# Kernel optimization log

Hardware: AMD Instinct MI355X
Metric: run time of the kernel (lower is better)

The kernel has to match this reference:

```python
import jax, jax.numpy as jnp
import numpy as np
from jax import lax

NE_RATIO = 0.8
SCALING_G = 1.0
W_FF = 30.0
SIG_EXT = 5.0
VT = 20.0
VR = 0.0
DT = 1e-3
NMAX = 60  # fixed Euler step count (Euler2fixedpt)
CONTRASTS = [0.0, 0.0432773, 0.103411, 0.186966, 0.303066, 0.464386, 0.68854, 1.0]
ORIENTS = [0., 15., 30., 45., 60., 75., 90., 105., 120., 135., 150., 165.]

# f_ricci polynomial coeffs in (-z), highest degree first (a9..a1, 0)
_FA = np.array([.14805913578876898, .64290613877355551, 1.0616084849547165,
                .93524391761244940, .62718906618071668, .32171431660633076,
                .32056016125642045, .77373949685442023, .22757881388024176, 0.0],
               dtype=np.float32)

def f_ricci(x):
    z = x / (1.0 + x)
    return jnp.log(2.0 * x + 1.0) + jnp.polyval(jnp.asarray(_FA), -z)

def g_ricci(x):
    z = x / (2.0 + x)
    num = z * (3.5441754117462949 + z * (-7.0529131065835378 + z * (-56.532378057580381
          + z * (279.56761105465944 + z * (-520.37554849441472 + z * (456.58245777026514
          + z * (-155.73340457809226)))))))
    den = 1.0 + z * (-4.1357968834226053 + z * (-7.2984226138266743 + z * (98.656602235468327
          + z * (-334.20436223415163 + z * (601.08633903294185 + z * (-599.58577549598340
          + z * (277.18420330693891 + z * (-16.445022798669722))))))))
    return num / den

def phi(mu, sigma, tau, tau_ref):
    """Ricciardi LIF transfer (Sanzeni rational approximation), branch-safe for jit."""
    xp = (mu - VR) / sigma
    xm = (mu - VT) / sigma
    cA = xm > 0
    cB = (xm <= 0) & (xp > 0)
    cC = xp <= 0
    xmA = jnp.where(cA, xm, 1.0); xpA = jnp.where(cA, xp, 2.0)
    rA = 1.0 / (f_ricci(xpA) - f_ricci(xmA))
    xmB = jnp.where(cB, xm, -1.0); xpB = jnp.where(cB, xp, 1.0)
    rB = 1.0 / (f_ricci(xpB) + jnp.exp(xmB * xmB) * g_ricci(-xmB))
    xmC = jnp.where(cC, xm, -2.0); xpC = jnp.where(cC, xp, -1.0)
    rC = jnp.exp(-xmC * xmC - jnp.log(g_ricci(-xmC) - jnp.exp(xpC * xpC - xmC * xmC) * g_ricci(-xpC)))
    r0 = jnp.where(cA, rA, jnp.where(cB, rB, rC))
    r0 = jnp.maximum(r0, 1e-30)
    return 1.0 / (tau_ref + tau / r0)

def _forward(hyperparameters, rand_mat, N):
    Ne = int(N * NE_RATIO); Ni = N - Ne
    pref = jnp.concatenate([
        jnp.linspace(0.0, 179.99, Ne, endpoint=False, dtype=jnp.float32),
        jnp.linspace(0.0, 179.99, Ni, endpoint=False, dtype=jnp.float32)])
    diff = jnp.abs(pref[:, None] - pref[None, :])              # [N,N]
    is_i = (jnp.arange(N) >= Ne).astype(jnp.int32)
    conn = is_i[:, None] + 2 * is_i[None, :]                   # 0:EE 1:IE 2:EI 3:II
    J = hyperparameters[0][conn]
    P = hyperparameters[1][conn]
    W = hyperparameters[2][conn]
    z = jnp.exp((jnp.cos(2.0 * jnp.pi / 180.0 * diff) - 1.0) / (4.0 * (jnp.pi / 180.0 * W) ** 2))
    weights = J * jax.nn.sigmoid(32.0 * (P * z - rand_mat))    # [N,N]
    weights2 = weights * weights
    tau = jnp.concatenate([0.01 * jnp.ones(Ne, jnp.float32), 0.01 * jnp.ones(Ni, jnp.float32)])
    T_inv = jnp.concatenate([100.0 * jnp.ones(Ne, jnp.float32), 200.0 * jnp.ones(Ni, jnp.float32)])
    tau_ref = jnp.concatenate([0.005 * jnp.ones(Ne, jnp.float32), 0.001 * jnp.ones(Ni, jnp.float32)])
    contrasts = jnp.asarray(CONTRASTS, jnp.float32)
    orients = jnp.asarray(ORIENTS, jnp.float32)
    dth = orients[None, :, None] - pref[None, None, :]         # [1,12,N]
    cg = jnp.exp((jnp.cos(2.0 * jnp.pi / 180.0 * dth) - 1.0) / (4.0 * (jnp.pi / 180.0 * W_FF) ** 2))
    mean = (contrasts[:, None, None] * 20.0 * SCALING_G * cg).reshape(-1, N)  # [96,N]
    sd2 = SIG_EXT * SIG_EXT

    def step(rate, _):
        mu = tau * (rate @ weights.T) + mean                   # [96,N]
        sig = jnp.sqrt(tau * (rate @ weights2.T) + sd2)
        rate = rate + DT * T_inv * (phi(mu, sig, tau, tau_ref) - rate)
        return rate, None

    rate, _ = lax.scan(step, jnp.zeros_like(mean), None, length=NMAX)
    all_rates = rate.reshape(len(CONTRASTS), len(ORIENTS), N)
    return jnp.transpose(all_rates, (2, 0, 1))                 # [N, 8, 12]

def setup_inputs():
    key = jax.random.key(0)
    hyperparameters = jnp.array([[1.99, 1.9, -1.01, -0.79],
                                 [0.11, 0.11, 0.45, 0.45],
                                 [32.0, 32.0, 32.0, 32.0]], dtype=jnp.float32)
    rand_mat = jax.random.uniform(key, (1500, 1500), dtype=jnp.float32)
    return {"hyperparameters": hyperparameters, "rand_mat": rand_mat, "neuron_num": 1500}

def reference(hyperparameters, rand_mat, neuron_num):
    return _forward(hyperparameters, rand_mat, neuron_num)
```

## Files before the change

kernel.cpp:

```cpp
#include <hip/hip_runtime.h>
#include <hip/hip_bf16.h>
#include <math.h>

#define NN      1500
#define NEE     1200
#define NPAD    1536
#define BATCH   96
#define NSTEP   60
#define PI_F    3.14159265358979323846f

#define NTHR    1024
#define WAVES   16
#define KSLW    (NPAD / WAVES)
#define BH      48
#define MFR     3

#define BP      49
#define SLOTF   (2 * 16 * BP)
#define LDS_BYTES (WAVES * SLOTF * 4)

typedef __attribute__((ext_vector_type(8))) short short8b;
typedef __attribute__((ext_vector_type(4))) float f32x4;


__device__ __forceinline__ ushort bf16_rn(float x) {
    unsigned u = __float_as_uint(x);
    unsigned r = (u + 0x7FFFu + ((u >> 16) & 1u)) >> 16;
    return (ushort)r;
}
__device__ __forceinline__ float bf16f(ushort h) {
    return __uint_as_float(((unsigned)h) << 16);
}


__device__ __forceinline__ float f_ricci(float x) {
    float z = x / (1.0f + x);
    float t = -z;
    float p = 0.14805913578876898f;
    p = p * t + 0.64290613877355551f;
    p = p * t + 1.0616084849547165f;
    p = p * t + 0.93524391761244940f;
    p = p * t + 0.62718906618071668f;
    p = p * t + 0.32171431660633076f;
    p = p * t + 0.32056016125642045f;
    p = p * t + 0.77373949685442023f;
    p = p * t + 0.22757881388024176f;
    p = p * t;
    return logf(2.0f * x + 1.0f) + p;
}

__device__ __forceinline__ float g_ricci(float x) {
    float z = x / (2.0f + x);
    float num = z * (3.5441754117462949f + z * (-7.0529131065835378f + z * (-56.532378057580381f
        + z * (279.56761105465944f + z * (-520.37554849441472f + z * (456.58245777026514f
        + z * (-155.73340457809226f)))))));
    float den = 1.0f + z * (-4.1357968834226053f + z * (-7.2984226138266743f + z * (98.656602235468327f
        + z * (-334.20436223415163f + z * (601.08633903294185f + z * (-599.58577549598340f
        + z * (277.18420330693891f + z * (-16.445022798669722f))))))));
    return num / den;
}

__device__ __forceinline__ float phi_lif(float mu, float sig, float tau, float tau_ref) {
    float xp = mu / sig;
    float xm = (mu - 20.0f) / sig;
    float r0;
    if (xm > 0.0f) {
        r0 = 1.0f / (f_ricci(xp) - f_ricci(xm));
    } else if (xp > 0.0f) {
        r0 = 1.0f / (f_ricci(xp) + expf(xm * xm) * g_ricci(-xm));
    } else {
        float a = g_ricci(-xm) - expf(xp * xp - xm * xm) * g_ricci(-xp);
        r0 = expf(-xm * xm - logf(a));
    }
    r0 = fmaxf(r0, 1e-30f);
    return 1.0f / (tau_ref + tau / r0);
}

__device__ __forceinline__ float pref_of(int n) {
    const float stepE = 179.99f / 1200.0f;
    const float stepI = 179.99f / 300.0f;
    return (n < NEE) ? (float)n * stepE : (float)(n - NEE) * stepI;
}


__global__ __launch_bounds__(256) void k_weights(const float* __restrict__ hyp,
        const float* __restrict__ rand_mat,
        ushort* __restrict__ Whi, ushort* __restrict__ Wlo,
        ushort* __restrict__ W2hi, ushort* __restrict__ W2lo) {
    int k = blockIdx.x * 256 + threadIdx.x;
    int i = blockIdx.y;
    size_t idx = (size_t)i * NPAD + k;
    if (i >= NN || k >= NN) {
        Whi[idx] = 0; Wlo[idx] = 0; W2hi[idx] = 0; W2lo[idx] = 0;
        return;
    }
    float diff = fabsf(pref_of(i) - pref_of(k));
    int conn = (i >= NEE ? 1 : 0) + 2 * (k >= NEE ? 1 : 0);
    float J  = hyp[conn];
    float P  = hyp[4 + conn];
    float Wp = hyp[8 + conn];
    float dn = 4.0f * (PI_F / 180.0f * Wp) * (PI_F / 180.0f * Wp);
    float z = expf((cosf(2.0f * PI_F / 180.0f * diff) - 1.0f) / dn);
    float x = 32.0f * (P * z - rand_mat[(size_t)i * NN + k]);
    float w = J / (1.0f + expf(-x));
    float w2 = w * w;
    ushort h = bf16_rn(w);
    Whi[idx] = h;  Wlo[idx] = bf16_rn(w - bf16f(h));
    ushort h2 = bf16_rn(w2);
    W2hi[idx] = h2; W2lo[idx] = bf16_rn(w2 - bf16f(h2));
}


__global__ __launch_bounds__(256) void k_init(float* __restrict__ mean,
                                              float* __restrict__ rate,
                                              ushort* __restrict__ rhiA,
                                              ushort* __restrict__ rloA) {
    int i = blockIdx.x * 256 + threadIdx.x;
    int b = blockIdx.y;
    int c = b / 12, o = b % 12;
    const float contrasts[8] = {0.0f, 0.0432773f, 0.103411f, 0.186966f,
                                0.303066f, 0.464386f, 0.68854f, 1.0f};
    float m = 0.0f;
    if (i < NN) {
        float dth = 15.0f * (float)o - pref_of(i);
        const float dn = 4.0f * (PI_F / 180.0f * 30.0f) * (PI_F / 180.0f * 30.0f);
        m = contrasts[c] * 20.0f * expf((cosf(2.0f * PI_F / 180.0f * dth) - 1.0f) / dn);
    }
    size_t idx = (size_t)b * NPAD + i;
    mean[idx] = m;
    rate[idx] = 0.0f;
    rhiA[idx] = 0;
    rloA[idx] = 0;
}


__global__ __launch_bounds__(NTHR) void k_step(
        const ushort* __restrict__ Whi, const ushort* __restrict__ Wlo,
        const ushort* __restrict__ W2hi, const ushort* __restrict__ W2lo,
        const ushort* __restrict__ rin_hi, const ushort* __restrict__ rin_lo,
        ushort* __restrict__ rout_hi, ushort* __restrict__ rout_lo,
        float* __restrict__ rate, const float* __restrict__ mean,
        float* __restrict__ out, int last)
{
    extern __shared__ float sm[];
    const int tid  = threadIdx.x;
    const int wave = tid >> 6;
    const int lane = tid & 63;
    const int lr   = lane & 15;
    const int lq   = lane >> 4;
    const int bx   = blockIdx.x;
    const int it   = bx % 96;
    const int bhf  = bx / 96;
    const int i0   = it * 16;
    const int b0   = bhf * BH;
    const int kb   = wave * KSLW;

    f32x4 acc1[MFR], acc2[MFR];
#pragma unroll
    for (int m = 0; m < MFR; m++) {
        acc1[m] = (f32x4){0.0f, 0.0f, 0.0f, 0.0f};
        acc2[m] = (f32x4){0.0f, 0.0f, 0.0f, 0.0f};
    }

    const size_t bof = (size_t)(i0 + lr) * NPAD + kb + lq * 8;
#pragma unroll
    for (int kk = 0; kk < KSLW / 32; kk++) {
        const int ko = kk * 32;
        short8b wh  = *(const short8b*)(Whi  + bof + ko);
        short8b wl  = *(const short8b*)(Wlo  + bof + ko);
        short8b w2h = *(const short8b*)(W2hi + bof + ko);
        short8b w2l = *(const short8b*)(W2lo + bof + ko);
#pragma unroll
        for (int m = 0; m < MFR; m++) {
            const size_t aof = (size_t)(b0 + m * 16 + lr) * NPAD + kb + lq * 8 + ko;
            short8b ah = *(const short8b*)(rin_hi + aof);
            short8b al = *(const short8b*)(rin_lo + aof);
            acc1[m] = __builtin_amdgcn_mfma_f32_16x16x32_bf16(ah, wh,  acc1[m], 0, 0, 0);
            acc1[m] = __builtin_amdgcn_mfma_f32_16x16x32_bf16(ah, wl,  acc1[m], 0, 0, 0);
            acc1[m] = __builtin_amdgcn_mfma_f32_16x16x32_bf16(al, wh,  acc1[m], 0, 0, 0);
            acc2[m] = __builtin_amdgcn_mfma_f32_16x16x32_bf16(ah, w2h, acc2[m], 0, 0, 0);
            acc2[m] = __builtin_amdgcn_mfma_f32_16x16x32_bf16(ah, w2l, acc2[m], 0, 0, 0);
            acc2[m] = __builtin_amdgcn_mfma_f32_16x16x32_bf16(al, w2h, acc2[m], 0, 0, 0);
        }
    }

    {
        float* sp = sm + wave * SLOTF;
#pragma unroll
        for (int m = 0; m < MFR; m++) {
            float* p1 = sp + lr * BP + m * 16 + 4 * lq;
            float* p2 = p1 + 16 * BP;
            *(f32x4*)p1 = acc1[m];
            *(f32x4*)p2 = acc2[m];
        }
    }
    __syncthreads();

    if (tid < BH * 16) {
        const int c = tid & 15;
        const int b = tid >> 4;
        const int ig = i0 + c;
        const int gb = b0 + b;
        const size_t gx = (size_t)gb * NPAD + ig;
        float rn = 0.0f;
        if (ig < NN) {
            float u1 = 0.0f, u2 = 0.0f;
#pragma unroll
            for (int s = 0; s < WAVES; s++) {
                u1 += sm[s * SLOTF + c * BP + b];
                u2 += sm[s * SLOTF + (16 + c) * BP + b];
            }
            float mu = 0.01f * u1 + mean[gx];
            float sg = sqrtf(0.01f * u2 + 25.0f);
            float tr = (ig < NEE) ? 0.005f : 0.001f;
            float Ti = (ig < NEE) ? 100.0f : 200.0f;
            float rr = rate[gx];
            float ph = phi_lif(mu, sg, 0.01f, tr);
            rn = rr + 1e-3f * Ti * (ph - rr);
            rate[gx] = rn;
            if (last) out[(size_t)ig * BATCH + gb] = rn;
        }
        ushort h = bf16_rn(rn);
        rout_hi[gx] = h;
        rout_lo[gx] = bf16_rn(rn - bf16f(h));
    }
}


extern "C" void kernel_launch(void* const* d_in, const int* in_sizes, int n_in,
                              void* d_out, int out_size, void* d_ws, size_t ws_size,
                              hipStream_t stream) {
    const float* hyp      = (const float*)d_in[0];
    const float* rand_mat = (const float*)d_in[1];
    float* out            = (float*)d_out;

    char* p = (char*)d_ws;
    ushort* Whi  = (ushort*)p; p += (size_t)NPAD * NPAD * 2;
    ushort* Wlo  = (ushort*)p; p += (size_t)NPAD * NPAD * 2;
    ushort* W2hi = (ushort*)p; p += (size_t)NPAD * NPAD * 2;
    ushort* W2lo = (ushort*)p; p += (size_t)NPAD * NPAD * 2;
    ushort* rhiA = (ushort*)p; p += (size_t)BATCH * NPAD * 2;
    ushort* rloA = (ushort*)p; p += (size_t)BATCH * NPAD * 2;
    ushort* rhiB = (ushort*)p; p += (size_t)BATCH * NPAD * 2;
    ushort* rloB = (ushort*)p; p += (size_t)BATCH * NPAD * 2;
    float*  mean = (float*)p;  p += (size_t)BATCH * NPAD * 4;
    float*  rate = (float*)p;  p += (size_t)BATCH * NPAD * 4;

    hipFuncSetAttribute((const void*)k_step,
                        hipFuncAttributeMaxDynamicSharedMemorySize, LDS_BYTES);

    k_weights<<<dim3(NPAD / 256, NPAD), 256, 0, stream>>>(hyp, rand_mat, Whi, Wlo, W2hi, W2lo);
    k_init<<<dim3(NPAD / 256, BATCH), 256, 0, stream>>>(mean, rate, rhiA, rloA);

    for (int s = 0; s < NSTEP; s++) {
        const ushort* ih = (s & 1) ? rhiB : rhiA;
        const ushort* il = (s & 1) ? rloB : rloA;
        ushort* oh = (s & 1) ? rhiA : rhiB;
        ushort* ol = (s & 1) ? rloA : rloB;
        k_step<<<dim3(192), dim3(NTHR), LDS_BYTES, stream>>>(
            Whi, Wlo, W2hi, W2lo, ih, il, oh, ol, rate, mean, out,
            (s == NSTEP - 1) ? 1 : 0);
    }
}
```

Before: 1.175 ms.

## Fuse all Euler steps into one cooperative persistent kernel with group barriers

Replaces the 60 per-step kernel launches with a single cooperative kernel that loops over steps. Workgroups handling the same batch half synchronise through an atomic counter barrier. The rate state and the mean input now live in registers instead of global arrays. Rate planes are read with relaxed agent-scope atomic loads and written as packed 32-bit atomic stores. This removes launch overhead and the per-step global traffic for rate and mean, at the cost of spin-wait barriers and weaker load vectorisation from the split 32-bit atomic loads.

After: 2.345 ms. 99.5% more time.

```diff
diff --git a/kernel.cpp b/kernel.cpp
--- a/kernel.cpp
+++ b/kernel.cpp
@@ -9,6 +9,8 @@
 #define NSTEP   60
 #define PI_F    3.14159265358979323846f
 
+#define NWG     192
+#define GRPWG   96
 #define NTHR    1024
 #define WAVES   16
 #define KSLW    (NPAD / WAVES)
@@ -30,6 +32,16 @@
 }
 __device__ __forceinline__ float bf16f(ushort h) {
     return __uint_as_float(((unsigned)h) << 16);
+}
+
+__device__ __forceinline__ short8b load_pair8(const ushort* plane, size_t elem) {
+    uint* p = (uint*)(plane + elem);
+    union { uint u[4]; short8b v; } x;
+    x.u[0] = __hip_atomic_load(p + 0, __ATOMIC_RELAXED, __HIP_MEMORY_SCOPE_AGENT);
+    x.u[1] = __hip_atomic_load(p + 1, __ATOMIC_RELAXED, __HIP_MEMORY_SCOPE_AGENT);
+    x.u[2] = __hip_atomic_load(p + 2, __ATOMIC_RELAXED, __HIP_MEMORY_SCOPE_AGENT);
+    x.u[3] = __hip_atomic_load(p + 3, __ATOMIC_RELAXED, __HIP_MEMORY_SCOPE_AGENT);
+    return x.v;
 }
 
 
@@ -111,36 +123,24 @@
 }
 
 
-__global__ __launch_bounds__(256) void k_init(float* __restrict__ mean,
-                                              float* __restrict__ rate,
-                                              ushort* __restrict__ rhiA,
-                                              ushort* __restrict__ rloA) {
+__global__ __launch_bounds__(256) void k_init(ushort* __restrict__ rhiA,
+                                              ushort* __restrict__ rloA,
+                                              uint* __restrict__ cnt) {
     int i = blockIdx.x * 256 + threadIdx.x;
     int b = blockIdx.y;
-    int c = b / 12, o = b % 12;
-    const float contrasts[8] = {0.0f, 0.0432773f, 0.103411f, 0.186966f,
-                                0.303066f, 0.464386f, 0.68854f, 1.0f};
-    float m = 0.0f;
-    if (i < NN) {
-        float dth = 15.0f * (float)o - pref_of(i);
-        const float dn = 4.0f * (PI_F / 180.0f * 30.0f) * (PI_F / 180.0f * 30.0f);
-        m = contrasts[c] * 20.0f * expf((cosf(2.0f * PI_F / 180.0f * dth) - 1.0f) / dn);
-    }
     size_t idx = (size_t)b * NPAD + i;
-    mean[idx] = m;
-    rate[idx] = 0.0f;
     rhiA[idx] = 0;
     rloA[idx] = 0;
-}
-
-
-__global__ __launch_bounds__(NTHR) void k_step(
+    if (blockIdx.x == 0 && blockIdx.y == 0 && threadIdx.x < 2) cnt[threadIdx.x] = 0;
+}
+
+
+__global__ __launch_bounds__(NTHR) void k_coop(
         const ushort* __restrict__ Whi, const ushort* __restrict__ Wlo,
         const ushort* __restrict__ W2hi, const ushort* __restrict__ W2lo,
-        const ushort* __restrict__ rin_hi, const ushort* __restrict__ rin_lo,
-        ushort* __restrict__ rout_hi, ushort* __restrict__ rout_lo,
-        float* __restrict__ rate, const float* __restrict__ mean,
-        float* __restrict__ out, int last)
+        ushort* __restrict__ rhiA, ushort* __restrict__ rloA,
+        ushort* __restrict__ rhiB, ushort* __restrict__ rloB,
+        uint* __restrict__ cnt, float* __restrict__ out)
 {
     extern __shared__ float sm[];
     const int tid  = threadIdx.x;
@@ -155,74 +155,115 @@
     const int b0   = bhf * BH;
     const int kb   = wave * KSLW;
 
-    f32x4 acc1[MFR], acc2[MFR];
-#pragma unroll
-    for (int m = 0; m < MFR; m++) {
-        acc1[m] = (f32x4){0.0f, 0.0f, 0.0f, 0.0f};
-        acc2[m] = (f32x4){0.0f, 0.0f, 0.0f, 0.0f};
+    const int c  = tid & 15;
+    const int bb = tid >> 4;
+    const int ig = i0 + c;
+    const int gb = b0 + bb;
+    const size_t gx = (size_t)gb * NPAD + ig;
+    const bool upd = (tid < BH * 16);
+
+    const float contrasts[8] = {0.0f, 0.0432773f, 0.103411f, 0.186966f,
+                                0.303066f, 0.464386f, 0.68854f, 1.0f};
+    const float dnff = 4.0f * (PI_F / 180.0f * 30.0f) * (PI_F / 180.0f * 30.0f);
+    float mean0 = 0.0f;
+    if (upd && ig < NN) {
+        float dth = 15.0f * (float)(gb % 12) - pref_of(ig);
+        mean0 = contrasts[gb / 12] * 20.0f *
+                expf((cosf(2.0f * PI_F / 180.0f * dth) - 1.0f) / dnff);
     }
+    float rr = 0.0f;
 
     const size_t bof = (size_t)(i0 + lr) * NPAD + kb + lq * 8;
-#pragma unroll
-    for (int kk = 0; kk < KSLW / 32; kk++) {
-        const int ko = kk * 32;
-        short8b wh  = *(const short8b*)(Whi  + bof + ko);
-        short8b wl  = *(const short8b*)(Wlo  + bof + ko);
-        short8b w2h = *(const short8b*)(W2hi + bof + ko);
-        short8b w2l = *(const short8b*)(W2lo + bof + ko);
+
+    for (int s = 0; s < NSTEP; s++) {
+        const ushort* rin_hi = (s & 1) ? rhiB : rhiA;
+        const ushort* rin_lo = (s & 1) ? rloB : rloA;
+        ushort* rout_hi = (s & 1) ? rhiA : rhiB;
+        ushort* rout_lo = (s & 1) ? rloA : rloB;
+
+        f32x4 acc1[MFR], acc2[MFR];
 #pragma unroll
         for (int m = 0; m < MFR; m++) {
-            const size_t aof = (size_t)(b0 + m * 16 + lr) * NPAD + kb + lq * 8 + ko;
-            short8b ah = *(const short8b*)(rin_hi + aof);
-            short8b al = *(const short8b*)(rin_lo + aof);
-            acc1[m] = __builtin_amdgcn_mfma_f32_16x16x32_bf16(ah, wh,  acc1[m], 0, 0, 0);
-            acc1[m] = __builtin_amdgcn_mfma_f32_16x16x32_bf16(ah, wl,  acc1[m], 0, 0, 0);
-            acc1[m] = __builtin_amdgcn_mfma_f32_16x16x32_bf16(al, wh,  acc1[m], 0, 0, 0);
-            acc2[m] = __builtin_amdgcn_mfma_f32_16x16x32_bf16(ah, w2h, acc2[m], 0, 0, 0);
-            acc2[m] = __builtin_amdgcn_mfma_f32_16x16x32_bf16(ah, w2l, acc2[m], 0, 0, 0);
-            acc2[m] = __builtin_amdgcn_mfma_f32_16x16x32_bf16(al, w2h, acc2[m], 0, 0, 0);
-        }
-    }
-
-    {
-        float* sp = sm + wave * SLOTF;
-#pragma unroll
-        for (int m = 0; m < MFR; m++) {
-            float* p1 = sp + lr * BP + m * 16 + 4 * lq;
-            float* p2 = p1 + 16 * BP;
-            *(f32x4*)p1 = acc1[m];
-            *(f32x4*)p2 = acc2[m];
-        }
-    }
-    __syncthreads();
-
-    if (tid < BH * 16) {
-        const int c = tid & 15;
-        const int b = tid >> 4;
-        const int ig = i0 + c;
-        const int gb = b0 + b;
-        const size_t gx = (size_t)gb * NPAD + ig;
-        float rn = 0.0f;
-        if (ig < NN) {
-            float u1 = 0.0f, u2 = 0.0f;
-#pragma unroll
-            for (int s = 0; s < WAVES; s++) {
-                u1 += sm[s * SLOTF + c * BP + b];
-                u2 += sm[s * SLOTF + (16 + c) * BP + b];
+            acc1[m] = (f32x4){0.0f, 0.0f, 0.0f, 0.0f};
+            acc2[m] = (f32x4){0.0f, 0.0f, 0.0f, 0.0f};
+        }
+
+#pragma unroll
+        for (int kk = 0; kk < KSLW / 32; kk++) {
+            const int ko = kk * 32;
+            short8b wh  = *(const short8b*)(Whi  + bof + ko);
+            short8b wl  = *(const short8b*)(Wlo  + bof + ko);
+            short8b w2h = *(const short8b*)(W2hi + bof + ko);
+            short8b w2l = *(const short8b*)(W2lo + bof + ko);
+#pragma unroll
+            for (int m = 0; m < MFR; m++) {
+                const size_t aof = (size_t)(b0 + m * 16 + lr) * NPAD + kb + lq * 8 + ko;
+                short8b ah = load_pair8(rin_hi, aof);
+                short8b al = load_pair8(rin_lo, aof);
+                acc1[m] = __builtin_amdgcn_mfma_f32_16x16x32_bf16(ah, wh,  acc1[m], 0, 0, 0);
+                acc1[m] = __builtin_amdgcn_mfma_f32_16x16x32_bf16(ah, wl,  acc1[m], 0, 0, 0);
+                acc1[m] = __builtin_amdgcn_mfma_f32_16x16x32_bf16(al, wh,  acc1[m], 0, 0, 0);
+                acc2[m] = __builtin_amdgcn_mfma_f32_16x16x32_bf16(ah, w2h, acc2[m], 0, 0, 0);
+                acc2[m] = __builtin_amdgcn_mfma_f32_16x16x32_bf16(ah, w2l, acc2[m], 0, 0, 0);
+                acc2[m] = __builtin_amdgcn_mfma_f32_16x16x32_bf16(al, w2h, acc2[m], 0, 0, 0);
             }
-            float mu = 0.01f * u1 + mean[gx];
-            float sg = sqrtf(0.01f * u2 + 25.0f);
-            float tr = (ig < NEE) ? 0.005f : 0.001f;
-            float Ti = (ig < NEE) ? 100.0f : 200.0f;
-            float rr = rate[gx];
-            float ph = phi_lif(mu, sg, 0.01f, tr);
-            rn = rr + 1e-3f * Ti * (ph - rr);
-            rate[gx] = rn;
-            if (last) out[(size_t)ig * BATCH + gb] = rn;
-        }
-        ushort h = bf16_rn(rn);
-        rout_hi[gx] = h;
-        rout_lo[gx] = bf16_rn(rn - bf16f(h));
+        }
+
+        {
+            float* sp = sm + wave * SLOTF;
+#pragma unroll
+            for (int m = 0; m < MFR; m++) {
+                float* p1 = sp + lr * BP + m * 16 + 4 * lq;
+                float* p2 = p1 + 16 * BP;
+                *(f32x4*)p1 = acc1[m];
+                *(f32x4*)p2 = acc2[m];
+            }
+        }
+        __syncthreads();
+
+        if (upd) {
+            float rn = 0.0f;
+            if (ig < NN) {
+                float u1 = 0.0f, u2 = 0.0f;
+#pragma unroll
+                for (int w = 0; w < WAVES; w++) {
+                    u1 += sm[w * SLOTF + c * BP + bb];
+                    u2 += sm[w * SLOTF + (16 + c) * BP + bb];
+                }
+                float mu = 0.01f * u1 + mean0;
+                float sg = sqrtf(0.01f * u2 + 25.0f);
+                float tr = (ig < NEE) ? 0.005f : 0.001f;
+                float Ti = (ig < NEE) ? 100.0f : 200.0f;
+                float ph = phi_lif(mu, sg, 0.01f, tr);
+                rr = rr + 1e-3f * Ti * (ph - rr);
+                rn = rr;
+                if (s == NSTEP - 1) out[(size_t)ig * BATCH + gb] = rn;
+            }
+            int hh = (int)bf16_rn(rn);
+            int ll = (int)bf16_rn(rn - bf16f((ushort)hh));
+            int hN = __shfl_down(hh, 1);
+            int lN = __shfl_down(ll, 1);
+            if ((c & 1) == 0) {
+                uint hp = (uint)hh | ((uint)hN << 16);
+                uint lp = (uint)ll | ((uint)lN << 16);
+                __hip_atomic_store((uint*)(rout_hi + gx), hp,
+                                   __ATOMIC_RELAXED, __HIP_MEMORY_SCOPE_AGENT);
+                __hip_atomic_store((uint*)(rout_lo + gx), lp,
+                                   __ATOMIC_RELAXED, __HIP_MEMORY_SCOPE_AGENT);
+            }
+        }
+
+        asm volatile("s_waitcnt vmcnt(0)" ::: "memory");
+        __syncthreads();
+        if (tid == 0) {
+            __hip_atomic_fetch_add(cnt + bhf, 1u,
+                                   __ATOMIC_RELAXED, __HIP_MEMORY_SCOPE_AGENT);
+            const uint target = (uint)(s + 1) * GRPWG;
+            while (__hip_atomic_load(cnt + bhf,
+                       __ATOMIC_RELAXED, __HIP_MEMORY_SCOPE_AGENT) < target)
+                __builtin_amdgcn_s_sleep(2);
+        }
+        __syncthreads();
     }
 }
 
@@ -243,22 +284,18 @@
     ushort* rloA = (ushort*)p; p += (size_t)BATCH * NPAD * 2;
     ushort* rhiB = (ushort*)p; p += (size_t)BATCH * NPAD * 2;
     ushort* rloB = (ushort*)p; p += (size_t)BATCH * NPAD * 2;
-    float*  mean = (float*)p;  p += (size_t)BATCH * NPAD * 4;
-    float*  rate = (float*)p;  p += (size_t)BATCH * NPAD * 4;
-
-    hipFuncSetAttribute((const void*)k_step,
+    uint*   cnt  = (uint*)p;   p += 256;
+
+    hipFuncSetAttribute((const void*)k_coop,
                         hipFuncAttributeMaxDynamicSharedMemorySize, LDS_BYTES);
 
-    k_weights<<<dim3(NPAD / 256, NPAD), 256, 0, stream>>>(hyp, rand_mat, Whi, Wlo, W2hi, W2lo);
-    k_init<<<dim3(NPAD / 256, BATCH), 256, 0, stream>>>(mean, rate, rhiA, rloA);
-
-    for (int s = 0; s < NSTEP; s++) {
-        const ushort* ih = (s & 1) ? rhiB : rhiA;
-        const ushort* il = (s & 1) ? rloB : rloA;
-        ushort* oh = (s & 1) ? rhiA : rhiB;
-        ushort* ol = (s & 1) ? rloA : rloB;
-        k_step<<<dim3(192), dim3(NTHR), LDS_BYTES, stream>>>(
-            Whi, Wlo, W2hi, W2lo, ih, il, oh, ol, rate, mean, out,
-            (s == NSTEP - 1) ? 1 : 0);
-    }
-}
+    k_weights<<<dim3(NPAD / 256, NPAD), 256, 0, stream>>>(hyp, rand_mat,
+                                                          Whi, Wlo, W2hi, W2lo);
+    k_init<<<dim3(NPAD / 256, BATCH), 256, 0, stream>>>(rhiA, rloA, cnt);
+
+    void* args[] = {(void*)&Whi, (void*)&Wlo, (void*)&W2hi, (void*)&W2lo,
+                    (void*)&rhiA, (void*)&rloA, (void*)&rhiB, (void*)&rloB,
+                    (void*)&cnt, (void*)&out};
+    hipLaunchCooperativeKernel((const void*)k_coop, dim3(NWG), dim3(NTHR),
+                               args, LDS_BYTES, stream);
+}
```
